# Optimization experiments

Hardware: AMD Instinct MI355X
Metric: run time of the kernel (lower is better)

Reference implementation:

```python
import jax, jax.numpy as jnp
import numpy as np

B, N, M = 16384, 2048, 2048


def setup_inputs() -> dict:
    key = jax.random.key(0)
    k1, k2 = jax.random.split(key, 2)
    X = jax.random.normal(k1, (B, N), dtype=jnp.float32)
    # master weights, kaiming-ish small scale
    W = jax.random.normal(k2, (M, N), dtype=jnp.float32) * 0.02
    bias = jnp.zeros((M,), dtype=jnp.float32)
    return {"X": X, "W": W, "bias": bias}


def reference(X, W, bias):
    # AbsMax ternary quantization: scale = max|W|, W_q = round(W/scale) clamped to {-1,0,1}
    scale = jnp.max(jnp.abs(W))
    W_ternary = jnp.clip(jnp.round(W / (scale + 1e-8)), -1.0, 1.0)
    # Y = X @ (W_ternary * scale)^T + bias   (the int32 bit-packing in the torch
    # code is computed but ignored by the dense F.linear, so it does not affect output)
    Y = X @ (W_ternary * scale).T + bias
    return Y
```

## Files before the change

### kernel.cpp

```cpp
#include <hip/hip_runtime.h>
#include <stdint.h>

typedef unsigned int uint32;

#define N_DIM 2048
#define M_DIM 2048
#define ROWS_PER_BLOCK 8
#define CAP 79
#define SLOTS 80
#define SLOTS_PAD 82
#define ZERO_ENTRY 32768u


__global__ __launch_bounds__(256) void k_absmax(const float* __restrict__ W,
                                                float* __restrict__ partials) {
    __shared__ float red[4];
    int tid = blockIdx.x * 256 + threadIdx.x;
    int stride = gridDim.x * 256;
    const float4* W4 = (const float4*)W;
    const int total4 = (M_DIM * N_DIM) / 4;
    float mx = 0.f;
    for (int i = tid; i < total4; i += stride) {
        float4 v = W4[i];
        mx = fmaxf(mx, fmaxf(fmaxf(fabsf(v.x), fabsf(v.y)),
                             fmaxf(fabsf(v.z), fabsf(v.w))));
    }
    for (int off = 32; off > 0; off >>= 1)
        mx = fmaxf(mx, __shfl_down(mx, off));
    if ((threadIdx.x & 63) == 0) red[threadIdx.x >> 6] = mx;
    __syncthreads();
    if (threadIdx.x == 0)
        partials[blockIdx.x] = fmaxf(fmaxf(red[0], red[1]), fmaxf(red[2], red[3]));
}

__global__ __launch_bounds__(256) void k_quant(const float* __restrict__ W,
                                               const float* __restrict__ partials,
                                               int* __restrict__ nnz,
                                               uint32* __restrict__ entries) {
    const int m    = (blockIdx.x * 256 + threadIdx.x) >> 6;
    const int lane = threadIdx.x & 63;
    const float4 pv = ((const float4*)partials)[lane];
    float mx = fmaxf(fmaxf(pv.x, pv.y), fmaxf(pv.z, pv.w));
#pragma unroll
    for (int off = 32; off > 0; off >>= 1)
        mx = fmaxf(mx, __shfl_xor(mx, off));
    const float s  = mx + 1e-8f;
    const float lo = 0.4999995f * s;
    const float hi = 0.5000005f * s;
    const float4* Wr4 = (const float4*)(W + (size_t)m * N_DIM);
    const unsigned long long lmask = (1ull << lane) - 1ull;
    int cnt = 0;
#pragma unroll
    for (int it = 0; it < N_DIM / 4 / 64; ++it) {
        const float4 v = Wr4[it * 64 + lane];
        const float w[4] = {v.x, v.y, v.z, v.w};
#pragma unroll
        for (int j = 0; j < 4; ++j) {
            const float a = fabsf(w[j]);
            bool nzf;
            if (a < lo)      nzf = false;
            else if (a > hi) nzf = true;
            else             nzf = (rintf(w[j] / s) != 0.f);
            const unsigned long long mask = __ballot(nzf);
            if (nzf) {
                const int slot = cnt + __popcll(mask & lmask);
                if (slot < CAP) {
                    const uint32 n = (uint32)((it * 64 + lane) * 4 + j);
                    const uint32 base  = n << 2;
                    const uint32 addrw = base ^ (((base >> 5) & 7) << 2);
                    entries[slot * M_DIM + m] = (addrw << 2) | (w[j] < 0.f ? 1u : 0u);
                }
            }
            cnt += __popcll(mask);
        }
    }
    const int c = cnt < CAP ? cnt : CAP;
    for (int s2 = c + lane; s2 < SLOTS; s2 += 64)
        entries[(size_t)s2 * M_DIM + m] = ZERO_ENTRY;
    if (lane == 0) nnz[m] = c;
}

__global__ __launch_bounds__(1024) void k_sort(const float* __restrict__ partials,
                                               const int* __restrict__ nnz,
                                               uint32* __restrict__ perm,
                                               uint32* __restrict__ rankS,
                                               uint32* __restrict__ scale_bits) {
    __shared__ int hist[SLOTS];
    __shared__ int base[SLOTS];
    const int t = threadIdx.x;
    if (t < SLOTS) hist[t] = 0;
    __syncthreads();
    if (t < 64) {
        const float4 pv = ((const float4*)partials)[t];
        float v = fmaxf(fmaxf(pv.x, pv.y), fmaxf(pv.z, pv.w));
#pragma unroll
        for (int off = 32; off > 0; off >>= 1)
            v = fmaxf(v, __shfl_down(v, off));
        if (t == 0) *scale_bits = __float_as_uint(v);
    }
    for (int i = t; i < M_DIM; i += 1024)
        atomicAdd(&hist[nnz[i]], 1);
    __syncthreads();
    if (t == 0) {
        int run = 0;
        for (int b = 0; b < SLOTS; ++b) { base[b] = run; run += hist[b]; }
    }
    __syncthreads();
    for (int i = t; i < M_DIM; i += 1024) {
        const int nz = nnz[i];
        const int pos = atomicAdd(&base[nz], 1);
        perm[pos] = ((uint32)nz << 16) | (uint32)i;
        rankS[i] = (uint32)((pos & ~511) | ((pos >> 3) & 63) | ((pos & 7) << 6));
    }
}

__global__ __launch_bounds__(256) void k_gather(const uint32* __restrict__ perm,
                                                const uint32* __restrict__ entries,
                                                uint32* __restrict__ entries_s,
                                                uint32* __restrict__ permS) {
    const int idx = blockIdx.x * 256 + threadIdx.x;
    const int i   = idx & (M_DIM - 1);
    const int s   = idx >> 11;
    const int q   = ((i & 63) << 3) | ((i >> 6) & 7) | (i & ~511);
    const uint32 pv = perm[q];
    const int m = (int)(pv & 0xffffu);
    entries_s[idx] = (s < SLOTS) ? entries[((size_t)s << 11) | (uint32)m] : ZERO_ENTRY;
    if (s == 0) permS[i] = pv;
}

__device__ __forceinline__ uint32 f2bf_rne(float f) {
    uint32 b = __float_as_uint(f);
    return (b + 0x7fffu + ((b >> 16) & 1u)) >> 16;
}

__global__ __launch_bounds__(512) void k_gemm(const float* __restrict__ X,
                                              const float* __restrict__ bias,
                                              const uint32* __restrict__ scale_bits,
                                              const uint32* __restrict__ permS,
                                              const uint32* __restrict__ rankS,
                                              const uint32* __restrict__ entries_s,
                                              float* __restrict__ Y) {
    __shared__ __align__(16) uint32 xs[N_DIM * 4 + 4];
    const int t = threadIdx.x;
    const int r0 = blockIdx.x * ROWS_PER_BLOCK;

    {
        const int u = t & 3;
        const int q = t >> 2;
        const float4* Xa = (const float4*)(X + (size_t)(r0 + 2 * u) * N_DIM);
        const float4* Xb = (const float4*)(X + (size_t)(r0 + 2 * u + 1) * N_DIM);
#pragma unroll
        for (int k = 0; k < 4; ++k) {
            const int c4 = q + (k << 7);
            const float4 va = Xa[c4];
            const float4 vb = Xb[c4];
            const float wa[4] = {va.x, va.y, va.z, va.w};
            const float wb[4] = {vb.x, vb.y, vb.z, vb.w};
#pragma unroll
            for (int i = 0; i < 4; ++i) {
                const uint32 packed = f2bf_rne(wa[i]) | (f2bf_rne(wb[i]) << 16);
                const int idx = (c4 << 4) + (i << 2) + u;
                xs[idx ^ (((idx >> 5) & 7) << 2)] = packed;
            }
        }
    }
    if (t < 4) xs[N_DIM * 4 + t] = 0u;
    __syncthreads();

    float acc[4][8];
#pragma unroll
    for (int j = 0; j < 4; ++j) {
        const int pos = t + (j << 9);
        const uint32 pw = permS[pos];
        const int wm = (int)(pw >> 16);
        const int wmax = __builtin_amdgcn_readfirstlane(__shfl(wm, 63));
#pragma unroll
        for (int r = 0; r < 8; ++r) acc[j][r] = 0.f;

        const uint32* ep = entries_s + pos;
        uint32 e0  = ep[0];
        uint32 e1  = ep[M_DIM];
        uint4  w0  = *(const uint4*)((const char*)xs + (e0 & 0xFFFFFFF0u));
        float  sg0 = __uint_as_float(0x3f800000u | (e0 << 31));
        for (int s = 0; s < wmax; ++s) {
            const uint32 e2  = ep[(size_t)(s + 2) * M_DIM];
            const uint4  w1  = *(const uint4*)((const char*)xs + (e1 & 0xFFFFFFF0u));
            const float  sg1 = __uint_as_float(0x3f800000u | (e1 << 31));
            acc[j][0] = fmaf(sg0, __uint_as_float(w0.x << 16),          acc[j][0]);
            acc[j][1] = fmaf(sg0, __uint_as_float(w0.x & 0xffff0000u),  acc[j][1]);
            acc[j][2] = fmaf(sg0, __uint_as_float(w0.y << 16),          acc[j][2]);
            acc[j][3] = fmaf(sg0, __uint_as_float(w0.y & 0xffff0000u),  acc[j][3]);
            acc[j][4] = fmaf(sg0, __uint_as_float(w0.z << 16),          acc[j][4]);
            acc[j][5] = fmaf(sg0, __uint_as_float(w0.z & 0xffff0000u),  acc[j][5]);
            acc[j][6] = fmaf(sg0, __uint_as_float(w0.w << 16),          acc[j][6]);
            acc[j][7] = fmaf(sg0, __uint_as_float(w0.w & 0xffff0000u),  acc[j][7]);
            e1 = e2; w0 = w1; sg0 = sg1;
        }
    }

    const float scale = __uint_as_float(*scale_bits);
    float4* res16 = (float4*)xs;
    uint32 rk[4];
    float  bb[4];
#pragma unroll
    for (int j = 0; j < 4; ++j) {
        rk[j] = rankS[t + (j << 9)];
        bb[j] = bias[t + (j << 9)];
    }
#pragma unroll
    for (int h = 0; h < 2; ++h) {
        __syncthreads();
#pragma unroll
        for (int j = 0; j < 4; ++j) {
            float4 v;
            v.x = acc[j][h * 4 + 0];
            v.y = acc[j][h * 4 + 1];
            v.z = acc[j][h * 4 + 2];
            v.w = acc[j][h * 4 + 3];
            res16[t + (j << 9)] = v;
        }
        __syncthreads();
#pragma unroll
        for (int j = 0; j < 4; ++j) {
            const float4 v = res16[rk[j]];
            const int m = t + (j << 9);
            float* Yp = Y + (size_t)(r0 + h * 4) * M_DIM + m;
            Yp[0 * M_DIM] = fmaf(scale, v.x, bb[j]);
            Yp[1 * M_DIM] = fmaf(scale, v.y, bb[j]);
            Yp[2 * M_DIM] = fmaf(scale, v.z, bb[j]);
            Yp[3 * M_DIM] = fmaf(scale, v.w, bb[j]);
        }
    }
}

extern "C" void kernel_launch(void* const* d_in, const int* in_sizes, int n_in,
                              void* d_out, int out_size, void* d_ws, size_t ws_size,
                              hipStream_t stream) {
    const float* X    = (const float*)d_in[0];
    const float* W    = (const float*)d_in[1];
    const float* bias = (const float*)d_in[2];
    float* Y = (float*)d_out;

    uint32* scale_bits = (uint32*)d_ws;
    float*  partials   = (float*)d_ws + 256;
    int*    nnz        = (int*)d_ws + 1024;
    uint32* perm       = (uint32*)d_ws + 3072;
    uint32* rankS      = (uint32*)d_ws + 5120;
    uint32* permS      = (uint32*)d_ws + 7168;
    uint32* entries    = (uint32*)d_ws + 10240;
    uint32* entries_s  = (uint32*)d_ws + 10240 + SLOTS * M_DIM;

    const int B = in_sizes[0] / N_DIM;

    hipLaunchKernelGGL(k_absmax, dim3(256),                     dim3(256),  0, stream, W, partials);
    hipLaunchKernelGGL(k_quant,  dim3(M_DIM * 64 / 256),        dim3(256),  0, stream, W, partials, nnz, entries);
    hipLaunchKernelGGL(k_sort,   dim3(1),                       dim3(1024), 0, stream, partials, nnz, perm, rankS, scale_bits);
    hipLaunchKernelGGL(k_gather, dim3(SLOTS_PAD * M_DIM / 256), dim3(256),  0, stream, perm, entries, entries_s, permS);
    hipLaunchKernelGGL(k_gemm,   dim3(B / ROWS_PER_BLOCK),      dim3(512),  0, stream,
                       X, bias, scale_bits, permS, rankS, entries_s, Y);
}
```

Baseline: 304.5 us.

## Balance per-wave work by pairing sorted row chunks and deepen the gather prefetch

The old interleaved permutation, which spread rows so that each wave got a mixed nnz profile, is removed. Rows stay in plain sorted order, and each wave takes chunks in reverse order for three of its j blocks and forward order for the last, which balances total slot iterations across the waves. The LDS prefetch pipeline goes from one lookahead to two, so more reads overlap with the FMAs. This adds register pressure and changes the result scatter indexing, which now uses posj.

```diff
diff --git a/kernel.cpp b/kernel.cpp
--- a/kernel.cpp
+++ b/kernel.cpp
@@ -110,7 +110,7 @@
         const int nz = nnz[i];
         const int pos = atomicAdd(&base[nz], 1);
         perm[pos] = ((uint32)nz << 16) | (uint32)i;
-        rankS[i] = (uint32)((pos & ~511) | ((pos >> 3) & 63) | ((pos & 7) << 6));
+        rankS[i] = (uint32)pos;
     }
 }
 
@@ -121,8 +121,7 @@
     const int idx = blockIdx.x * 256 + threadIdx.x;
     const int i   = idx & (M_DIM - 1);
     const int s   = idx >> 11;
-    const int q   = ((i & 63) << 3) | ((i >> 6) & 7) | (i & ~511);
-    const uint32 pv = perm[q];
+    const uint32 pv = perm[i];
     const int m = (int)(pv & 0xffffu);
     entries_s[idx] = (s < SLOTS) ? entries[((size_t)s << 11) | (uint32)m] : ZERO_ENTRY;
     if (s == 0) permS[i] = pv;
@@ -167,10 +166,15 @@
     if (t < 4) xs[N_DIM * 4 + t] = 0u;
     __syncthreads();
 
+    const int wv = t >> 6;
+    const int ln = t & 63;
     float acc[4][8];
+    int   posj[4];
 #pragma unroll
     for (int j = 0; j < 4; ++j) {
-        const int pos = t + (j << 9);
+        const int wb  = (j < 3) ? (7 - wv) : wv;
+        const int pos = (j << 9) + (wb << 6) + ln;
+        posj[j] = pos;
         const uint32 pw = permS[pos];
         const int wm = (int)(pw >> 16);
         const int wmax = __builtin_amdgcn_readfirstlane(__shfl(wm, 63));
@@ -178,23 +182,25 @@
         for (int r = 0; r < 8; ++r) acc[j][r] = 0.f;
 
         const uint32* ep = entries_s + pos;
-        uint32 e0  = ep[0];
-        uint32 e1  = ep[M_DIM];
-        uint4  w0  = *(const uint4*)((const char*)xs + (e0 & 0xFFFFFFF0u));
-        float  sg0 = __uint_as_float(0x3f800000u | (e0 << 31));
+        uint32 e0 = ep[0];
+        uint32 e1 = ep[M_DIM];
+        uint32 e2 = ep[2 * M_DIM];
+        uint4  w0 = *(const uint4*)((const char*)xs + (e0 & 0xFFFFFFF0u));
+        uint4  w1 = *(const uint4*)((const char*)xs + (e1 & 0xFFFFFFF0u));
         for (int s = 0; s < wmax; ++s) {
-            const uint32 e2  = ep[(size_t)(s + 2) * M_DIM];
-            const uint4  w1  = *(const uint4*)((const char*)xs + (e1 & 0xFFFFFFF0u));
-            const float  sg1 = __uint_as_float(0x3f800000u | (e1 << 31));
-            acc[j][0] = fmaf(sg0, __uint_as_float(w0.x << 16),          acc[j][0]);
-            acc[j][1] = fmaf(sg0, __uint_as_float(w0.x & 0xffff0000u),  acc[j][1]);
-            acc[j][2] = fmaf(sg0, __uint_as_float(w0.y << 16),          acc[j][2]);
-            acc[j][3] = fmaf(sg0, __uint_as_float(w0.y & 0xffff0000u),  acc[j][3]);
-            acc[j][4] = fmaf(sg0, __uint_as_float(w0.z << 16),          acc[j][4]);
-            acc[j][5] = fmaf(sg0, __uint_as_float(w0.z & 0xffff0000u),  acc[j][5]);
-            acc[j][6] = fmaf(sg0, __uint_as_float(w0.w << 16),          acc[j][6]);
-            acc[j][7] = fmaf(sg0, __uint_as_float(w0.w & 0xffff0000u),  acc[j][7]);
-            e1 = e2; w0 = w1; sg0 = sg1;
+            const uint32 e3 = ep[(size_t)(s + 3) * M_DIM];
+            const uint4  w2 = *(const uint4*)((const char*)xs + (e2 & 0xFFFFFFF0u));
+            const float  sg = __uint_as_float(0x3f800000u | (e0 << 31));
+            acc[j][0] = fmaf(sg, __uint_as_float(w0.x << 16),          acc[j][0]);
+            acc[j][1] = fmaf(sg, __uint_as_float(w0.x & 0xffff0000u),  acc[j][1]);
+            acc[j][2] = fmaf(sg, __uint_as_float(w0.y << 16),          acc[j][2]);
+            acc[j][3] = fmaf(sg, __uint_as_float(w0.y & 0xffff0000u),  acc[j][3]);
+            acc[j][4] = fmaf(sg, __uint_as_float(w0.z << 16),          acc[j][4]);
+            acc[j][5] = fmaf(sg, __uint_as_float(w0.z & 0xffff0000u),  acc[j][5]);
+            acc[j][6] = fmaf(sg, __uint_as_float(w0.w << 16),          acc[j][6]);
+            acc[j][7] = fmaf(sg, __uint_as_float(w0.w & 0xffff0000u),  acc[j][7]);
+            e0 = e1; e1 = e2; e2 = e3;
+            w0 = w1; w1 = w2;
         }
     }
 
@@ -217,7 +223,7 @@
             v.y = acc[j][h * 4 + 1];
             v.z = acc[j][h * 4 + 2];
             v.w = acc[j][h * 4 + 3];
-            res16[t + (j << 9)] = v;
+            res16[posj[j]] = v;
         }
         __syncthreads();
 #pragma unroll
```

Result: faster. 286.0 us (-6.1%).
